# Performance work log

Hardware: AMD Instinct MI355X
Metric: run time of the kernel (lower is better)

The kernel has to match this reference:

```python
import math
import jax, jax.numpy as jnp
import numpy as np

B, T, C = 4, 2048, 1024
N_HEAD = 16
HEAD_DIM = C // N_HEAD

def setup_inputs() -> dict:
    key = jax.random.key(0)
    k0, k1, k2, k3, k4 = jax.random.split(key, 5)
    s = 1.0 / math.sqrt(C)
    return {
        "x": jax.random.normal(k0, (B, T, C), dtype=jnp.float32),
        "W_q": jax.random.normal(k1, (C, C), dtype=jnp.float32) * s,
        "W_k": jax.random.normal(k2, (C, C), dtype=jnp.float32) * s,
        "W_v": jax.random.normal(k3, (C, C), dtype=jnp.float32) * s,
        "W_o": jax.random.normal(k4, (C, C), dtype=jnp.float32) * s,
    }

def reference(x, W_q, W_k, W_v, W_o):
    b, t, c = x.shape
    h, hd = N_HEAD, HEAD_DIM
    # nn.Linear(y) = y @ W.T ; project and split heads -> [B, H, T, hd]
    q = (x @ W_q.T).reshape(b, t, h, hd).transpose(0, 2, 1, 3)
    k = (x @ W_k.T).reshape(b, t, h, hd).transpose(0, 2, 1, 3)
    v = (x @ W_v.T).reshape(b, t, h, hd).transpose(0, 2, 1, 3)
    # scores [B, H, T, T], causal mask, stable softmax
    attn = jnp.einsum('bhqd,bhkd->bhqk', q, k) / math.sqrt(hd)
    causal = jnp.tril(jnp.ones((t, t), dtype=bool))
    attn = jnp.where(causal[None, None], attn, -jnp.inf)
    attn = jax.nn.softmax(attn, axis=-1)
    out = jnp.einsum('bhqk,bhkd->bhqd', attn, v)
    out = out.transpose(0, 2, 1, 3).reshape(b, t, c)
    return out @ W_o.T
```

## Files before the change

kernel.cpp:

```cpp
#include <hip/hip_runtime.h>
#include <math.h>

#define Bsz 4
#define Tsz 2048
#define Csz 1024
#define NH  16
#define HD  64

typedef short bf16x8 __attribute__((ext_vector_type(8)));
typedef float f32x4  __attribute__((ext_vector_type(4)));
typedef unsigned short u16;
typedef unsigned int uint;

__device__ __forceinline__ u16 f2bf(float f) {
    union { float f; unsigned u; } v; v.f = f;
    unsigned r = v.u + 0x7fffu + ((v.u >> 16) & 1u);
    return (u16)(r >> 16);
}

__device__ __forceinline__ uint pkbf(float a, float b) {
    union { float f; uint u; } x, y; x.f = a; y.f = b;
    return ((x.u + 0x8000u) >> 16) | ((y.u + 0x8000u) & 0xFFFF0000u);
}

__device__ __forceinline__ void glds16(const u16* g, u16* l) {
    __builtin_amdgcn_global_load_lds(
        (const __attribute__((address_space(1))) void*)g,
        (__attribute__((address_space(3))) void*)l, 16, 0, 0);
}

__global__ void cast_kernel(const float* __restrict__ src, u16* __restrict__ dst, int n) {
    int i = (blockIdx.x * blockDim.x + threadIdx.x) * 8;
    if (i + 8 <= n) {
        float4 a = *(const float4*)(src + i);
        float4 b = *(const float4*)(src + i + 4);
        bf16x8 o;
        o[0] = (short)f2bf(a.x); o[1] = (short)f2bf(a.y);
        o[2] = (short)f2bf(a.z); o[3] = (short)f2bf(a.w);
        o[4] = (short)f2bf(b.x); o[5] = (short)f2bf(b.y);
        o[6] = (short)f2bf(b.z); o[7] = (short)f2bf(b.w);
        *(bf16x8*)(dst + i) = o;
    } else {
        for (; i < n; i++) dst[i] = f2bf(src[i]);
    }
}

__global__ void cast4_kernel(const float* __restrict__ s0, const float* __restrict__ s1,
                             const float* __restrict__ s2, const float* __restrict__ s3,
                             u16* __restrict__ dst) {
    const int NW = Csz * Csz;
    int i = (blockIdx.x * blockDim.x + threadIdx.x) * 8;
    int m = i >> 20;
    int local = i & (NW - 1);
    const float* src = (m == 0) ? s0 : (m == 1) ? s1 : (m == 2) ? s2 : s3;
    float4 a = *(const float4*)(src + local);
    float4 b = *(const float4*)(src + local + 4);
    bf16x8 o;
    o[0] = (short)f2bf(a.x); o[1] = (short)f2bf(a.y);
    o[2] = (short)f2bf(a.z); o[3] = (short)f2bf(a.w);
    o[4] = (short)f2bf(b.x); o[5] = (short)f2bf(b.y);
    o[6] = (short)f2bf(b.z); o[7] = (short)f2bf(b.w);
    *(bf16x8*)(dst + i) = o;
}

#define GEMM_PIPELINE_BODY(A_, B_, K_)                                               \
    __shared__ u16 sA[2][128 * 32];                                                  \
    __shared__ u16 sB[2][128 * 32];                                                  \
    const int tid  = threadIdx.x;                                                    \
    const int wave = tid >> 6, lane = tid & 63;                                      \
    const int lr = lane & 15, lq = lane >> 4;                                        \
    const int m0 = blockIdx.y * 128, n0 = blockIdx.x * 128;                          \
    const int wm = (wave & 1) * 64, wn = (wave >> 1) * 64;                           \
    const int srow = lane >> 2;                                                      \
    const int scol = (lane & 3) * 8;                                                 \
    const u16* gA = (A_) + (size_t)(m0 + wave * 32 + srow) * (K_) + scol;            \
    const u16* gB = (B_) + (size_t)(n0 + wave * 32 + srow) * (K_) + scol;            \
    f32x4 acc[4][4] = {};                                                            \
    {                                                                                \
        u16* dA = &sA[0][0] + wave * 1024;                                           \
        u16* dB = &sB[0][0] + wave * 1024;                                           \
        glds16(gA, dA);                                                              \
        glds16(gA + (size_t)16 * (K_), dA + 512);                                    \
        glds16(gB, dB);                                                              \
        glds16(gB + (size_t)16 * (K_), dB + 512);                                    \
    }                                                                                \
    int buf = 0;                                                                     \
    for (int k0 = 0; k0 < (K_); k0 += 32) {                                          \
        __syncthreads();                                                             \
        if (k0 + 32 < (K_)) {                                                        \
            u16* dA = &sA[buf ^ 1][0] + wave * 1024;                                 \
            u16* dB = &sB[buf ^ 1][0] + wave * 1024;                                 \
            glds16(gA + k0 + 32, dA);                                                \
            glds16(gA + (size_t)16 * (K_) + k0 + 32, dA + 512);                      \
            glds16(gB + k0 + 32, dB);                                                \
            glds16(gB + (size_t)16 * (K_) + k0 + 32, dB + 512);                      \
        }                                                                            \
        const u16* rA = &sA[buf][0];                                                 \
        const u16* rB = &sB[buf][0];                                                 \
        bf16x8 af[4], bfv[4];                                                        \
        _Pragma("unroll")                                                            \
        for (int f = 0; f < 4; f++)                                                  \
            af[f]  = *(const bf16x8*)(rA + (wm + f * 16 + lr) * 32 + lq * 8);        \
        _Pragma("unroll")                                                            \
        for (int f = 0; f < 4; f++)                                                  \
            bfv[f] = *(const bf16x8*)(rB + (wn + f * 16 + lr) * 32 + lq * 8);        \
        _Pragma("unroll")                                                            \
        for (int i = 0; i < 4; i++)                                                  \
            _Pragma("unroll")                                                        \
            for (int j = 0; j < 4; j++)                                              \
                acc[i][j] = __builtin_amdgcn_mfma_f32_16x16x32_bf16(af[i], bfv[j], acc[i][j], 0, 0, 0); \
        buf ^= 1;                                                                    \
    }

__global__ __launch_bounds__(256, 2)
void gemm_qkv(const u16* __restrict__ A, const u16* __restrict__ Bm,
              u16* __restrict__ Qo, u16* __restrict__ Ko, u16* __restrict__ Vo,
              float qscale) {
    GEMM_PIPELINE_BODY(A, Bm, Csz)

    const int sel = n0 >> 10;
    if (sel == 2) {
        #pragma unroll
        for (int i = 0; i < 4; i++) {
            #pragma unroll
            for (int j = 0; j < 4; j++) {
                int m = m0 + wm + i * 16 + lq * 4;
                int b = m >> 11, t = m & (Tsz - 1);
                int n = (n0 & 1023) + wn + j * 16 + lr;
                int h = n >> 6, d = n & (HD - 1);
                uint2 pk;
                pk.x = pkbf(acc[i][j][0], acc[i][j][1]);
                pk.y = pkbf(acc[i][j][2], acc[i][j][3]);
                *(uint2*)(&Vo[(((size_t)b * NH + h) * HD + d) * Tsz + t]) = pk;
            }
        }
    } else {
        const float scale = (sel == 0) ? qscale : 1.0f;
        u16* dst = (sel == 0) ? Qo : Ko;
        #pragma unroll
        for (int i = 0; i < 4; i++)
            #pragma unroll
            for (int j = 0; j < 4; j++)
                #pragma unroll
                for (int r = 0; r < 4; r++) {
                    int m = m0 + wm + i * 16 + lq * 4 + r;
                    int n = (n0 & 1023) + wn + j * 16 + lr;
                    int b = m >> 11, t = m & (Tsz - 1);
                    int h = n >> 6,  d = n & (HD - 1);
                    dst[(((size_t)b * NH + h) * Tsz + t) * HD + d] = f2bf(acc[i][j][r] * scale);
                }
    }
}

__global__ __launch_bounds__(256, 2)
void gemm_out(const u16* __restrict__ A, const u16* __restrict__ Bm,
              float* __restrict__ out) {
    GEMM_PIPELINE_BODY(A, Bm, Csz)

    #pragma unroll
    for (int i = 0; i < 4; i++)
        #pragma unroll
        for (int j = 0; j < 4; j++)
            #pragma unroll
            for (int r = 0; r < 4; r++) {
                int m = m0 + wm + i * 16 + lq * 4 + r;
                int n = n0 + wn + j * 16 + lr;
                out[(size_t)m * Csz + n] = acc[i][j][r];
            }
}

#define LDT  72
#define LDTP 68

__global__ __launch_bounds__(256, 4)
void attn_kernel(const u16* __restrict__ Q, const u16* __restrict__ Kb,
                 const u16* __restrict__ Vt, u16* __restrict__ O) {
    __shared__ u16 sK[64 * LDT];
    __shared__ u16 sV[64 * LDT];
    __shared__ u16 sP[4][16 * LDTP];
    const int tid  = threadIdx.x;
    const int wave = tid >> 6, lane = tid & 63;
    const int lr = lane & 15, lq = lane >> 4;
    const int bh = blockIdx.x;
    const int qa = blockIdx.y;
    const int qc = 31 - qa;
    const int ta = qa * 64, tc = qc * 64;

    const u16* Qp = Q  + (size_t)bh * Tsz * HD;
    const u16* Kp = Kb + (size_t)bh * Tsz * HD;
    const u16* Vp = Vt + (size_t)bh * HD * Tsz;

    bf16x8 qfA0 = *(const bf16x8*)(Qp + (size_t)(ta + wave * 16 + lr) * HD + lq * 8);
    bf16x8 qfA1 = *(const bf16x8*)(Qp + (size_t)(ta + wave * 16 + lr) * HD + 32 + lq * 8);
    bf16x8 qfC0 = *(const bf16x8*)(Qp + (size_t)(tc + wave * 16 + lr) * HD + lq * 8);
    bf16x8 qfC1 = *(const bf16x8*)(Qp + (size_t)(tc + wave * 16 + lr) * HD + 32 + lq * 8);

    f32x4 accOA[4] = {}, accOC[4] = {};
    f32x4 accLA = {}, accLC = {};

    bf16x8 ones;
    #pragma unroll
    for (int i = 0; i < 8; i++) ones[i] = (short)0x3F80;

    const int strow = tid >> 3;
    const int stcol = (tid & 7) * 8;
    const u16* gK0 = Kp + (size_t)strow * HD + stcol;
    const u16* gK1 = gK0 + 32 * HD;
    const u16* gV0 = Vp + (size_t)strow * Tsz + stcol;
    const u16* gV1 = gV0 + 32 * Tsz;
    u16* lK0 = sK + strow * LDT + stcol;  u16* lK1 = lK0 + 32 * LDT;
    u16* lV0 = sV + strow * LDT + stcol;  u16* lV1 = lV0 + 32 * LDT;

    bf16x8 pK0 = *(const bf16x8*)(gK0);
    bf16x8 pK1 = *(const bf16x8*)(gK1);
    bf16x8 pV0 = *(const bf16x8*)(gV0);
    bf16x8 pV1 = *(const bf16x8*)(gV1);

#define PROCESS(T0, QF0, QF1, ACCO, ACCL, DIAG)                                       \
    {                                                                                 \
        f32x4 accS[4];                                                                \
        _Pragma("unroll")                                                             \
        for (int j = 0; j < 4; j++) {                                                 \
            bf16x8 b0 = *(const bf16x8*)(sK + (j * 16 + lr) * LDT + lq * 8);          \
            bf16x8 b1 = *(const bf16x8*)(sK + (j * 16 + lr) * LDT + 32 + lq * 8);     \
            f32x4 z = {};                                                             \
            z = __builtin_amdgcn_mfma_f32_16x16x32_bf16(QF0, b0, z, 0, 0, 0);         \
            z = __builtin_amdgcn_mfma_f32_16x16x32_bf16(QF1, b1, z, 0, 0, 0);         \
            accS[j] = z;                                                              \
        }                                                                             \
        _Pragma("unroll")                                                             \
        for (int r = 0; r < 4; r++) {                                                 \
            const int rowg = (T0) + wave * 16 + lq * 4 + r;                           \
            _Pragma("unroll")                                                         \
            for (int j = 0; j < 4; j++) {                                             \
                float v = accS[j][r];                                                 \
                if (DIAG && (kb * 64 + j * 16 + lr > rowg)) v = -200.0f;              \
                union { float f; uint u; } e;                                         \
                e.f = __builtin_amdgcn_exp2f(v);                                      \
                sP[wave][(lq * 4 + r) * LDTP + j * 16 + lr] = (u16)(e.u >> 16);       \
            }                                                                         \
        }                                                                             \
        _Pragma("unroll")                                                             \
        for (int ks = 0; ks < 2; ks++) {                                              \
            bf16x8 pf = *(const bf16x8*)(&sP[wave][0] + lr * LDTP + ks * 32 + lq * 8);\
            ACCL = __builtin_amdgcn_mfma_f32_16x16x32_bf16(pf, ones, ACCL, 0, 0, 0);  \
            _Pragma("unroll")                                                         \
            for (int j = 0; j < 4; j++) {                                             \
                bf16x8 vf = *(const bf16x8*)(sV + (j * 16 + lr) * LDT + ks * 32 + lq * 8); \
                ACCO[j] = __builtin_amdgcn_mfma_f32_16x16x32_bf16(pf, vf, ACCO[j], 0, 0, 0); \
            }                                                                         \
        }                                                                             \
    }

    for (int kb = 0; kb <= qc; kb++) {
        __syncthreads();
        *(bf16x8*)lK0 = pK0; *(bf16x8*)lK1 = pK1;
        *(bf16x8*)lV0 = pV0; *(bf16x8*)lV1 = pV1;
        __syncthreads();
        if (kb < qc) {
            pK0 = *(const bf16x8*)(gK0 + (size_t)(kb + 1) * 64 * HD);
            pK1 = *(const bf16x8*)(gK1 + (size_t)(kb + 1) * 64 * HD);
            pV0 = *(const bf16x8*)(gV0 + (kb + 1) * 64);
            pV1 = *(const bf16x8*)(gV1 + (kb + 1) * 64);
        }
        if (kb <= qa) PROCESS(ta, qfA0, qfA1, accOA, accLA, (kb == qa));
        PROCESS(tc, qfC0, qfC1, accOC, accLC, (kb == qc));
    }
#undef PROCESS

    const int b = bh >> 4, h = bh & 15;
    #pragma unroll
    for (int j = 0; j < 4; j++) {
        #pragma unroll
        for (int r = 0; r < 4; r++) {
            int t = wave * 16 + lq * 4 + r;
            int d = j * 16 + lr;
            O[((size_t)b * Tsz + ta + t) * Csz + h * HD + d] = f2bf(accOA[j][r] / accLA[r]);
            O[((size_t)b * Tsz + tc + t) * Csz + h * HD + d] = f2bf(accOC[j][r] / accLC[r]);
        }
    }
}

extern "C" void kernel_launch(void* const* d_in, const int* in_sizes, int n_in,
                              void* d_out, int out_size, void* d_ws, size_t ws_size,
                              hipStream_t stream) {
    const float* x  = (const float*)d_in[0];
    const float* Wq = (const float*)d_in[1];
    const float* Wk = (const float*)d_in[2];
    const float* Wv = (const float*)d_in[3];
    const float* Wo = (const float*)d_in[4];
    float* out = (float*)d_out;

    const size_t NX = (size_t)Bsz * Tsz * Csz;
    const size_t NW = (size_t)Csz * Csz;

    char* ws = (char*)d_ws;
    u16* xb   = (u16*)ws; ws += NX * 2;
    u16* wqkv = (u16*)ws; ws += 3 * NW * 2;
    u16* wob  = (u16*)ws; ws += NW * 2;
    u16* qbuf = (u16*)ws; ws += NX * 2;
    u16* kbuf = (u16*)ws; ws += NX * 2;
    u16* vtb  = (u16*)ws; ws += NX * 2;
    u16* abuf = (u16*)ws; ws += NX * 2;

    cast_kernel<<<dim3((unsigned)(NX / 2048)), 256, 0, stream>>>(x, xb, (int)NX);
    cast4_kernel<<<dim3((unsigned)(4 * NW / 2048)), 256, 0, stream>>>(Wq, Wk, Wv, Wo, wqkv);

    const float qscale = 0.125f * 1.44269504088896340736f;
    gemm_qkv<<<dim3(24, 64), 256, 0, stream>>>(xb, wqkv, qbuf, kbuf, vtb, qscale);

    attn_kernel<<<dim3(Bsz * NH, 16), 256, 0, stream>>>(qbuf, kbuf, vtb, abuf);

    gemm_out<<<dim3(8, 64), 256, 0, stream>>>(abuf, wob, out);
}
```

Baseline: 258.3 us.

## Rewrite projection GEMMs with 256x256 tiles, swizzled LDS, and split-phase pipelining

Both projection GEMMs move from 128x128 tiles on 256 threads to 256x256 tiles on 512 threads with 8 waves. K is split into 64-wide steps, each done as four half-phases, with explicit vmcnt waits and prefetch of the next stages interleaved. LDS loads use an XOR swizzle to avoid bank conflicts, and s_setprio is raised around the MFMA blocks. Block indices are remapped into chunked groups for L2 locality. The costs are 128 KB of LDS per block and more accumulator registers, which may limit occupancy, and the QKV grid of 384 blocks may quantize poorly over the CUs.

```diff
diff --git a/kernel.cpp b/kernel.cpp
--- a/kernel.cpp
+++ b/kernel.cpp
@@ -63,109 +63,145 @@
     *(bf16x8*)(dst + i) = o;
 }
 
-#define GEMM_PIPELINE_BODY(A_, B_, K_)                                               \
-    __shared__ u16 sA[2][128 * 32];                                                  \
-    __shared__ u16 sB[2][128 * 32];                                                  \
-    const int tid  = threadIdx.x;                                                    \
-    const int wave = tid >> 6, lane = tid & 63;                                      \
-    const int lr = lane & 15, lq = lane >> 4;                                        \
-    const int m0 = blockIdx.y * 128, n0 = blockIdx.x * 128;                          \
-    const int wm = (wave & 1) * 64, wn = (wave >> 1) * 64;                           \
-    const int srow = lane >> 2;                                                      \
-    const int scol = (lane & 3) * 8;                                                 \
-    const u16* gA = (A_) + (size_t)(m0 + wave * 32 + srow) * (K_) + scol;            \
-    const u16* gB = (B_) + (size_t)(n0 + wave * 32 + srow) * (K_) + scol;            \
-    f32x4 acc[4][4] = {};                                                            \
+
+#define G8_SLOTSZ 32768
+#define G8_MATSZ  16384
+#define G8_KHSZ    8192
+
+#define G8_STAGE(SLOT, MAT, KH, KT, PTR)                                             \
+    { _Pragma("unroll")                                                              \
+      for (int rho = 0; rho < 2; rho++) {                                            \
+        const int row = rho * 128 + (tid >> 2);                                      \
+        const int sc = (tid & 3) ^ ((row >> 1) & 3);                                 \
+        glds16((PTR) + (size_t)row * 1024 + (KT) * 64 + (KH) * 32 + sc * 8,          \
+               lds + (SLOT) * G8_SLOTSZ + (MAT) * G8_MATSZ + (KH) * G8_KHSZ +        \
+                     rho * 4096 + wave * 512);                                       \
+    } }
+
+#define G8_PHASE(SLOT, KH, MH, STAGE)                                                \
     {                                                                                \
-        u16* dA = &sA[0][0] + wave * 1024;                                           \
-        u16* dB = &sB[0][0] + wave * 1024;                                           \
-        glds16(gA, dA);                                                              \
-        glds16(gA + (size_t)16 * (K_), dA + 512);                                    \
-        glds16(gB, dB);                                                              \
-        glds16(gB + (size_t)16 * (K_), dB + 512);                                    \
-    }                                                                                \
-    int buf = 0;                                                                     \
-    for (int k0 = 0; k0 < (K_); k0 += 32) {                                          \
-        __syncthreads();                                                             \
-        if (k0 + 32 < (K_)) {                                                        \
-            u16* dA = &sA[buf ^ 1][0] + wave * 1024;                                 \
-            u16* dB = &sB[buf ^ 1][0] + wave * 1024;                                 \
-            glds16(gA + k0 + 32, dA);                                                \
-            glds16(gA + (size_t)16 * (K_) + k0 + 32, dA + 512);                      \
-            glds16(gB + k0 + 32, dB);                                                \
-            glds16(gB + (size_t)16 * (K_) + k0 + 32, dB + 512);                      \
+        __builtin_amdgcn_s_barrier();                                                \
+        asm volatile("" ::: "memory");                                               \
+        STAGE                                                                        \
+        const u16* abase = lds + (SLOT) * G8_SLOTSZ + (KH) * G8_KHSZ;                \
+        const u16* bbase = abase + G8_MATSZ;                                         \
+        if ((MH) == 0) {                                                             \
+            _Pragma("unroll")                                                        \
+            for (int j = 0; j < 4; j++) {                                            \
+                const int nr = wcb + j * 16 + lr;                                    \
+                bfrag[j] = *(const bf16x8*)(bbase + nr * 32 +                        \
+                                            ((lq ^ ((nr >> 1) & 3)) * 8));           \
+            }                                                                        \
         }                                                                            \
-        const u16* rA = &sA[buf][0];                                                 \
-        const u16* rB = &sB[buf][0];                                                 \
-        bf16x8 af[4], bfv[4];                                                        \
+        bf16x8 afr[4];                                                               \
         _Pragma("unroll")                                                            \
-        for (int f = 0; f < 4; f++)                                                  \
-            af[f]  = *(const bf16x8*)(rA + (wm + f * 16 + lr) * 32 + lq * 8);        \
-        _Pragma("unroll")                                                            \
-        for (int f = 0; f < 4; f++)                                                  \
-            bfv[f] = *(const bf16x8*)(rB + (wn + f * 16 + lr) * 32 + lq * 8);        \
+        for (int i = 0; i < 4; i++) {                                                \
+            const int ar = wrb + ((MH) * 4 + i) * 16 + lr;                           \
+            afr[i] = *(const bf16x8*)(abase + ar * 32 +                              \
+                                      ((lq ^ ((ar >> 1) & 3)) * 8));                 \
+        }                                                                            \
+        asm volatile("" ::: "memory");                                               \
+        __builtin_amdgcn_s_setprio(1);                                               \
         _Pragma("unroll")                                                            \
         for (int i = 0; i < 4; i++)                                                  \
             _Pragma("unroll")                                                        \
             for (int j = 0; j < 4; j++)                                              \
-                acc[i][j] = __builtin_amdgcn_mfma_f32_16x16x32_bf16(af[i], bfv[j], acc[i][j], 0, 0, 0); \
-        buf ^= 1;                                                                    \
-    }
-
-__global__ __launch_bounds__(256, 2)
+                acc[(MH) * 4 + i][j] = __builtin_amdgcn_mfma_f32_16x16x32_bf16(      \
+                    afr[i], bfrag[j], acc[(MH) * 4 + i][j], 0, 0, 0);                \
+        __builtin_amdgcn_s_setprio(0);                                               \
+    }
+
+#define G8_VM(N) asm volatile("s_waitcnt vmcnt(" #N ")" ::: "memory")
+
+#define G8_BODY(AP_, BP_)                                                            \
+    __shared__ u16 lds[65536];                                                       \
+    const int tid = threadIdx.x;                                                     \
+    const int wave = tid >> 6, lane = tid & 63;                                      \
+    const int lr = lane & 15, lq = lane >> 4;                                        \
+    const int wrb = (wave >> 2) * 128, wcb = (wave & 3) * 64;                        \
+    f32x4 acc[8][4] = {};                                                            \
+    bf16x8 bfrag[4];                                                                 \
+    G8_STAGE(0, 0, 0, 0, AP_) G8_STAGE(0, 1, 0, 0, BP_)                              \
+    G8_STAGE(0, 0, 1, 0, AP_) G8_STAGE(0, 1, 1, 0, BP_)                              \
+    G8_STAGE(1, 0, 0, 1, AP_) G8_STAGE(1, 1, 0, 1, BP_)                              \
+    for (int t = 0; t < 16; t++) {                                                   \
+        const int s = t & 1;                                                         \
+        if (t == 15) { G8_VM(4); } else { G8_VM(8); }                                \
+        G8_PHASE(s, 0, 0, if (t < 15) G8_STAGE(s ^ 1, 0, 1, t + 1, AP_))             \
+        G8_PHASE(s, 0, 1, if (t < 15) G8_STAGE(s ^ 1, 1, 1, t + 1, BP_))             \
+        if (t == 15) { G8_VM(0); } else { G8_VM(8); }                                \
+        G8_PHASE(s, 1, 0, if (t < 14) G8_STAGE(s, 0, 0, t + 2, AP_))                 \
+        G8_PHASE(s, 1, 1, if (t < 14) G8_STAGE(s, 1, 0, t + 2, BP_))                 \
+    }
+
+__global__ __launch_bounds__(512, 2)
 void gemm_qkv(const u16* __restrict__ A, const u16* __restrict__ Bm,
               u16* __restrict__ Qo, u16* __restrict__ Ko, u16* __restrict__ Vo,
               float qscale) {
-    GEMM_PIPELINE_BODY(A, Bm, Csz)
+    const int wg = blockIdx.x;
+    const int chunk = wg & 7, pos = wg >> 3;
+    const int m0 = ((chunk >> 1) * 8 + pos / 6) * 256;
+    const int n0 = ((chunk & 1) * 6 + pos % 6) * 256;
+    const u16* Ap = A  + (size_t)m0 * 1024;
+    const u16* Bp = Bm + (size_t)n0 * 1024;
+
+    G8_BODY(Ap, Bp)
 
     const int sel = n0 >> 10;
     if (sel == 2) {
         #pragma unroll
-        for (int i = 0; i < 4; i++) {
+        for (int mi = 0; mi < 8; mi++) {
             #pragma unroll
-            for (int j = 0; j < 4; j++) {
-                int m = m0 + wm + i * 16 + lq * 4;
-                int b = m >> 11, t = m & (Tsz - 1);
-                int n = (n0 & 1023) + wn + j * 16 + lr;
+            for (int ni = 0; ni < 4; ni++) {
+                int m = m0 + wrb + mi * 16 + lq * 4;
+                int b = m >> 11, tt = m & (Tsz - 1);
+                int n = (n0 & 1023) + wcb + ni * 16 + lr;
                 int h = n >> 6, d = n & (HD - 1);
                 uint2 pk;
-                pk.x = pkbf(acc[i][j][0], acc[i][j][1]);
-                pk.y = pkbf(acc[i][j][2], acc[i][j][3]);
-                *(uint2*)(&Vo[(((size_t)b * NH + h) * HD + d) * Tsz + t]) = pk;
+                pk.x = pkbf(acc[mi][ni][0], acc[mi][ni][1]);
+                pk.y = pkbf(acc[mi][ni][2], acc[mi][ni][3]);
+                *(uint2*)(&Vo[(((size_t)b * NH + h) * HD + d) * Tsz + tt]) = pk;
             }
         }
     } else {
         const float scale = (sel == 0) ? qscale : 1.0f;
         u16* dst = (sel == 0) ? Qo : Ko;
         #pragma unroll
-        for (int i = 0; i < 4; i++)
+        for (int mi = 0; mi < 8; mi++)
             #pragma unroll
-            for (int j = 0; j < 4; j++)
+            for (int ni = 0; ni < 4; ni++)
                 #pragma unroll
                 for (int r = 0; r < 4; r++) {
-                    int m = m0 + wm + i * 16 + lq * 4 + r;
-                    int n = (n0 & 1023) + wn + j * 16 + lr;
-                    int b = m >> 11, t = m & (Tsz - 1);
+                    int m = m0 + wrb + mi * 16 + lq * 4 + r;
+                    int n = (n0 & 1023) + wcb + ni * 16 + lr;
+                    int b = m >> 11, tt = m & (Tsz - 1);
                     int h = n >> 6,  d = n & (HD - 1);
-                    dst[(((size_t)b * NH + h) * Tsz + t) * HD + d] = f2bf(acc[i][j][r] * scale);
+                    dst[(((size_t)b * NH + h) * Tsz + tt) * HD + d] = f2bf(acc[mi][ni][r] * scale);
                 }
     }
 }
 
-__global__ __launch_bounds__(256, 2)
+__global__ __launch_bounds__(512, 2)
 void gemm_out(const u16* __restrict__ A, const u16* __restrict__ Bm,
               float* __restrict__ out) {
-    GEMM_PIPELINE_BODY(A, Bm, Csz)
+    const int wg = blockIdx.x;
+    const int chunk = wg & 7, pos = wg >> 3;
+    const int m0 = (chunk * 4 + (pos >> 2)) * 256;
+    const int n0 = (pos & 3) * 256;
+    const u16* Ap = A  + (size_t)m0 * 1024;
+    const u16* Bp = Bm + (size_t)n0 * 1024;
+
+    G8_BODY(Ap, Bp)
 
     #pragma unroll
-    for (int i = 0; i < 4; i++)
+    for (int mi = 0; mi < 8; mi++)
         #pragma unroll
-        for (int j = 0; j < 4; j++)
+        for (int ni = 0; ni < 4; ni++)
             #pragma unroll
             for (int r = 0; r < 4; r++) {
-                int m = m0 + wm + i * 16 + lq * 4 + r;
-                int n = n0 + wn + j * 16 + lr;
-                out[(size_t)m * Csz + n] = acc[i][j][r];
+                int m = m0 + wrb + mi * 16 + lq * 4 + r;
+                int n = n0 + wcb + ni * 16 + lr;
+                out[(size_t)m * Csz + n] = acc[mi][ni][r];
             }
 }
 
@@ -307,9 +343,9 @@
     cast4_kernel<<<dim3((unsigned)(4 * NW / 2048)), 256, 0, stream>>>(Wq, Wk, Wv, Wo, wqkv);
 
     const float qscale = 0.125f * 1.44269504088896340736f;
-    gemm_qkv<<<dim3(24, 64), 256, 0, stream>>>(xb, wqkv, qbuf, kbuf, vtb, qscale);
+    gemm_qkv<<<dim3(384), 512, 0, stream>>>(xb, wqkv, qbuf, kbuf, vtb, qscale);
 
     attn_kernel<<<dim3(Bsz * NH, 16), 256, 0, stream>>>(qbuf, kbuf, vtb, abuf);
 
-    gemm_out<<<dim3(8, 64), 256, 0, stream>>>(abuf, wob, out);
-}
+    gemm_out<<<dim3(128), 512, 0, stream>>>(abuf, wob, out);
+}
```

New measurement: 251.7 us. 1.03x faster.
